# Performance work log

Hardware: AMD Instinct MI355X
Metric: run time of the kernel (lower is better)

Reference implementation:

```python
import jax, jax.numpy as jnp
import numpy as np

E, B, T, DIN, D = 8, 16, 512, 256, 256  # ensemble, batch, seq, input_dim, d_model*factor


def setup_inputs() -> dict:
    key = jax.random.key(0)
    ks = jax.random.split(key, 9)
    s_in = 1.0 / np.sqrt(DIN)
    s_d = 1.0 / np.sqrt(D)
    return {
        "x": jax.random.normal(ks[0], (E, B, T, DIN), jnp.float32),
        "hidden": jnp.zeros((1, E * B, 2 * D), jnp.float32),
        "rnn_start": (jax.random.uniform(ks[1], (B, T, 1)) < 0.02).astype(jnp.float32),
        "W_in": jax.random.normal(ks[2], (2, E, DIN, D), jnp.float32) * s_in,
        "b_in": jax.random.normal(ks[3], (2, E, D), jnp.float32) * 0.01,
        "W_mid": jax.random.normal(ks[4], (4, E, D, D), jnp.float32) * s_d,
        "b_mid": jax.random.normal(ks[5], (4, E, D), jnp.float32) * 0.01,
        "W_out": jax.random.normal(ks[6], (E, D, D), jnp.float32) * s_d,
        "b_out": jax.random.normal(ks[7], (E, D), jnp.float32) * 0.01,
    }


def _scan_tie_input_gate(v, f, h0):
    # h_t = f_t * h_{t-1} + (1 - f_t) * v_t  (tied input gate), via associative scan.
    # v, f: [N, T, D]; h0: [N, 1, D]
    b = (1.0 - f) * v

    def combine(x, y):
        a1, b1 = x
        a2, b2 = y
        return a1 * a2, a2 * b1 + b2

    A, Bc = jax.lax.associative_scan(combine, (f, b), axis=1)
    out = A * h0 + Bc  # [N, T, D]
    return out, out[:, -1:, :]


def reference(x, hidden, rnn_start, W_in, b_in, W_mid, b_mid, W_out, b_out):
    # --- first GILR stage ---
    u = jnp.einsum('ebti,meio->mebto', x, W_in) + b_in[:, :, None, None, :]
    v = jnp.tanh(u[0])
    f = jax.nn.sigmoid(u[1])
    f = f * (1.0 - rnn_start)[None]  # rnn_start [B,T,1] broadcasts over E, D

    vr = v.reshape(E * B, T, D)
    fr = f.reshape(E * B, T, D)

    h_pre, h_mid = jnp.split(hidden, 2, axis=-1)          # each [1, E*B, D]
    h_pre = jnp.transpose(h_pre, (1, 0, 2))               # [E*B, 1, D]
    h_mid = jnp.transpose(h_mid, (1, 0, 2))

    vr, h_pre_last = _scan_tie_input_gate(vr, fr, h_pre)
    v4 = vr.reshape(E, B, T, D)

    # --- LSTM-like middle stage ---
    u = jnp.einsum('ebti,meio->mebto', v4, W_mid) + b_mid[:, :, None, None, :]
    f = jax.nn.sigmoid(u[0])
    i = jax.nn.sigmoid(u[1])
    o = jax.nn.sigmoid(u[2])
    z = jnp.tanh(u[3])
    f = f * (1.0 - rnn_start)[None]

    fr = f.reshape(E * B, T, D)
    izr = (i * z).reshape(E * B, T, D)
    orr = o.reshape(E * B, T, D)

    out, h_mid_last = _scan_tie_input_gate(izr, fr, h_mid)
    out = out * orr
    out4 = out.reshape(E, B, T, D)

    # --- output projection ---
    out4 = jnp.einsum('ebti,eio->ebto', out4, W_out) + b_out[:, None, None, :]

    hidden_out = jnp.transpose(jnp.concatenate([h_pre_last, h_mid_last], axis=-1), (1, 0, 2))
    return out4, hidden_out
```

## Files before the change

### kernel.cpp

```cpp
#include <hip/hip_runtime.h>
#include <hip/hip_bf16.h>
#include <stdint.h>
#include <stddef.h>


typedef __bf16 bf16x8 __attribute__((ext_vector_type(8)));
typedef __bf16 bf16x4 __attribute__((ext_vector_type(4)));
typedef __bf16 bf16x2 __attribute__((ext_vector_type(2)));
typedef float  f32x4  __attribute__((ext_vector_type(4)));
typedef float  f32x2  __attribute__((ext_vector_type(2)));
typedef unsigned int u32x2 __attribute__((ext_vector_type(2)));

#define E_ 8
#define M_ 8192
#define K_ 256

__device__ __forceinline__ float sigm_f(float x) {
    return __builtin_amdgcn_rcpf(1.0f + __expf(-x));
}
__device__ __forceinline__ float tanh_f(float x) {
    return 1.0f - 2.0f * __builtin_amdgcn_rcpf(1.0f + __expf(2.0f * x));
}

__device__ __forceinline__ void g2lds16(const void* g, void* l) {
    __builtin_amdgcn_global_load_lds((const __attribute__((address_space(1))) void*)g,
                                     (__attribute__((address_space(3))) void*)l, 16, 0, 0);
}

template <int D>
__device__ __forceinline__ float dppshr(float x) {
    return __builtin_bit_cast(float,
        __builtin_amdgcn_update_dpp(0, __builtin_bit_cast(int, x),
                                    0x110 | D, 0xF, 0xF, true));
}

__device__ __forceinline__ void lane_scan(float& A, float& B, float& EA, float& EB, int ln15) {
    float As, Bs;
    Bs = dppshr<1>(B); As = dppshr<1>(A); B = __builtin_fmaf(A, Bs, B); A = (ln15 >= 1) ? A * As : A;
    Bs = dppshr<2>(B); As = dppshr<2>(A); B = __builtin_fmaf(A, Bs, B); A = (ln15 >= 2) ? A * As : A;
    Bs = dppshr<4>(B); As = dppshr<4>(A); B = __builtin_fmaf(A, Bs, B); A = (ln15 >= 4) ? A * As : A;
    Bs = dppshr<8>(B); As = dppshr<8>(A); B = __builtin_fmaf(A, Bs, B); A = (ln15 >= 8) ? A * As : A;
    EA = dppshr<1>(A); EA = (ln15 >= 1) ? EA : 1.0f;
    EB = dppshr<1>(B);
}

__global__ __launch_bounds__(256) void convx_k(const float* __restrict__ x, __bf16* __restrict__ xb) {
    int i = blockIdx.x * 256 + threadIdx.x;
    float4 v = ((const float4*)x)[i];
    bf16x4 o;
    o[0] = (__bf16)v.x; o[1] = (__bf16)v.y; o[2] = (__bf16)v.z; o[3] = (__bf16)v.w;
    ((bf16x4*)xb)[i] = o;
}

__global__ __launch_bounds__(256) void transw_k(const float* __restrict__ src, __bf16* __restrict__ dst,
                                                int NG, int ilv) {
    int ge = blockIdx.z;
    int g = ge >> 3, e = ge & 7;
    int k0 = blockIdx.x * 64, d0 = blockIdx.y * 64;
    __shared__ float tile[64][65];
    int t = threadIdx.x;
#pragma unroll
    for (int j = 0; j < 16; ++j) {
        int lin = j * 256 + t;
        int r = lin >> 6, c = lin & 63;
        tile[r][c] = src[((size_t)(ge * 256 + k0 + r)) * 256 + d0 + c];
    }
    __syncthreads();
#pragma unroll
    for (int j = 0; j < 16; ++j) {
        int lin = j * 256 + t;
        int r = lin >> 6, c = lin & 63;
        int d = d0 + r;
        int row = ilv ? (d * NG + g) : (g * 256 + d);
        dst[((size_t)(e * NG * 256 + row)) * K_ + k0 + c] = (__bf16)tile[c][r];
    }
}

template <int MODE, int NG>
__global__ __launch_bounds__(512, 1) void gemm_k(const __bf16* __restrict__ A,
                                                 const __bf16* __restrict__ Wt,
                                                 const float* __restrict__ bias,
                                                 const float* __restrict__ rs,
                                                 __bf16* __restrict__ gout,
                                                 float* __restrict__ fout,
                                                 const float* __restrict__ hidden,
                                                 float* __restrict__ hidout) {
    constexpr int NT  = NG * 2;
    constexpr int NMT = 2 * NT;
    const int tid = threadIdx.x;
    const int bid = blockIdx.x;
    const int e  = bid & 7;
    const int rr = bid >> 3;
    const int nt = rr & (NT - 1);
    const int ms = rr / NT;
    const int mt0 = ms * NMT;
    const int lane = tid & 63, wid = tid >> 6;
    const int wr = wid >> 2, wc = wid & 3;
    const int ln15 = lane & 15, ln16 = lane >> 4;

    __shared__ __align__(16) __bf16 As[2][32768];
    __shared__ float cAl[64], cBl[64];
    __shared__ float chL[2][64];

    bf16x8 Breg[2][8];
    {
        const __bf16* bp = Wt + ((size_t)e * (NG * 256) + nt * 128 + wc * 32 + ln15) * K_ + ln16 * 8;
#pragma unroll
        for (int j = 0; j < 2; ++j)
#pragma unroll
            for (int s = 0; s < 8; ++s)
                Breg[j][s] = *(const bf16x8*)(bp + (size_t)j * 16 * K_ + s * 32);
    }
    f32x4 bias_v[2];
#pragma unroll
    for (int j = 0; j < 2; ++j) {
        int n0 = nt * 128 + wc * 32 + j * 16 + (ln16 << 2);
        if constexpr (MODE == 0) {
#pragma unroll
            for (int q = 0; q < 4; ++q) {
                int n = n0 + q;
                bias_v[j][q] = bias[((n & 1) * E_ + e) * 256 + (n >> 1)];
            }
        } else if constexpr (MODE == 1) {
#pragma unroll
            for (int q = 0; q < 4; ++q) {
                int n = n0 + q;
                bias_v[j][q] = bias[((n & 3) * E_ + e) * 256 + (n >> 2)];
            }
        } else {
            bias_v[j] = *(const f32x4*)&bias[e * 256 + n0];
        }
    }

    const size_t Ae = ((size_t)e * M_ + (size_t)mt0 * 128) * K_;
    const int sr = tid >> 5, sr2 = sr >> 2;
    const int gg0 = (tid & 31) ^ sr2;
    const __bf16* sE = A + Ae + (size_t)sr * K_ + gg0 * 8;
    const __bf16* sO = A + Ae + (size_t)sr * K_ + (gg0 ^ 4) * 8;
    __bf16* const dbase0 = &As[0][tid * 8];
    __bf16* const dbase1 = &As[1][tid * 8];

    auto stage = [&](int tt, int buf) {
        __bf16* d = buf ? dbase1 : dbase0;
        const size_t toff = (size_t)tt * (128 * K_);
#pragma unroll
        for (int q = 0; q < 8; ++q)
            g2lds16(((q & 1) ? sO : sE) + toff + q * (16 * K_), d + q * 4096);
    };

    const int rowb = (wr * 64 + ln15 * 4) * K_;
    const int gb = ln16 ^ (lane & 7);
    const int pe_off = rowb + gb * 8;
    const int po_off = rowb + (gb ^ 4) * 8;

    f32x4 acc[4][2] = {};

    auto compute = [&](int buf) {
        const __bf16* pe = &As[0][0] + buf * 32768 + pe_off;
        const __bf16* po = &As[0][0] + buf * 32768 + po_off;
#pragma unroll
        for (int s = 0; s < 8; ++s) {
            const __bf16* p = (s & 1) ? po : pe;
            bf16x8 af[4];
#pragma unroll
            for (int i = 0; i < 4; ++i)
                af[i] = *(const bf16x8*)(p + i * K_ + (s >> 1) * 64);
#pragma unroll
            for (int i = 0; i < 4; ++i)
#pragma unroll
                for (int j = 0; j < 2; ++j)
                    acc[i][j] = __builtin_amdgcn_mfma_f32_16x16x32_bf16(Breg[j][s], af[i], acc[i][j], 0, 0, 0);
        }
    };

    stage(0, 0);
    asm volatile("s_waitcnt vmcnt(0)" ::: "memory");
    __builtin_amdgcn_s_barrier();
    __builtin_amdgcn_sched_barrier(0);

    int buf = 0;
    for (int t = 0; t < NMT; ++t) {
        const bool cs = ((t & 3) == 0);
        const int c = t >> 2;
        f32x4 rs4 = {};
        float hidv[4] = {0.f, 0.f, 0.f, 0.f};
        if constexpr (MODE != 2) {
            const int mbh = (mt0 + t) * 128 + wr * 64 + ln15 * 4;
            rs4 = *(const f32x4*)&rs[mbh];
            if constexpr (MODE == 1) {
                const int nrow = e * 16 + ms * 4 + c;
                hidv[0] = hidden[nrow * 512 + 256 + (nt * 32 + wc * 8 + 0 + ln16)];
                hidv[1] = hidden[nrow * 512 + 256 + (nt * 32 + wc * 8 + 4 + ln16)];
            } else {
                const int nrow = e * 16 + ms * 2 + c;
                f32x2 ha = *(const f32x2*)&hidden[nrow * 512 + (nt * 64 + wc * 16 + 0 + ln16 * 2)];
                f32x2 hb = *(const f32x2*)&hidden[nrow * 512 + (nt * 64 + wc * 16 + 8 + ln16 * 2)];
                hidv[0] = ha[0]; hidv[1] = ha[1]; hidv[2] = hb[0]; hidv[3] = hb[1];
            }
            __builtin_amdgcn_sched_barrier(0);
        }

        if (t + 1 < NMT) stage(t + 1, buf ^ 1);
        compute(buf);

        const int mt = mt0 + t;
        const int mb = mt * 128 + wr * 64 + ln15 * 4;

        if constexpr (MODE == 2) {
#pragma unroll
            for (int j = 0; j < 2; ++j) {
                const int n0 = nt * 128 + wc * 32 + j * 16 + (ln16 << 2);
#pragma unroll
                for (int i = 0; i < 4; ++i) {
                    f32x4 o = acc[i][j] + bias_v[j];
                    *(f32x4*)&fout[((size_t)e * M_ + mb + i) * 256 + n0] = o;
                    acc[i][j] = f32x4{};
                }
            }
        } else {
            f32x4 rsv;
#pragma unroll
            for (int q = 0; q < 4; ++q) rsv[q] = 1.0f - rs4[q];

            if constexpr (MODE == 1) {
                float PA[2][4], PB[2][4], Ov[2][4], LA[2], LB[2], EA[2], EB[2];
#pragma unroll
                for (int j = 0; j < 2; ++j) {
#pragma unroll
                    for (int i = 0; i < 4; ++i) {
                        float f  = sigm_f(acc[i][j][0] + bias_v[j][0]) * rsv[i];
                        float iv = sigm_f(acc[i][j][1] + bias_v[j][1]);
                        float o  = sigm_f(acc[i][j][2] + bias_v[j][2]);
                        float z  = tanh_f(acc[i][j][3] + bias_v[j][3]);
                        float b  = (1.0f - f) * iv * z;
                        Ov[j][i] = o;
                        if (i == 0) { PA[j][0] = f; PB[j][0] = b; }
                        else { PB[j][i] = __builtin_fmaf(f, PB[j][i - 1], b); PA[j][i] = PA[j][i - 1] * f; }
                        acc[i][j] = f32x4{};
                    }
                    LA[j] = PA[j][3]; LB[j] = PB[j][3];
                    lane_scan(LA[j], LB[j], EA[j], EB[j], ln15);
                }
                if (wr == 0 && ln15 == 15) {
#pragma unroll
                    for (int j = 0; j < 2; ++j) {
                        int sl = wc * 8 + j * 4 + ln16;
                        cAl[sl] = LA[j]; cBl[sl] = LB[j];
                    }
                }
                asm volatile("s_waitcnt lgkmcnt(0)" ::: "memory");
                __builtin_amdgcn_s_barrier();
#pragma unroll
                for (int j = 0; j < 2; ++j) {
                    const int sl = wc * 8 + j * 4 + ln16;
                    const int d = nt * 32 + wc * 8 + j * 4 + ln16;
                    float hp = cs ? hidv[j] : chL[t & 1][sl];
                    float hs = wr ? __builtin_fmaf(cAl[sl], hp, cBl[sl]) : hp;
                    float h0 = __builtin_fmaf(EA[j], hs, EB[j]);
#pragma unroll
                    for (int i = 0; i < 4; ++i) {
                        float h = __builtin_fmaf(PA[j][i], h0, PB[j][i]);
                        gout[((size_t)e * M_ + mb + i) * 256 + d] = (__bf16)(h * Ov[j][i]);
                    }
                    if (wr == 1 && ln15 == 15) {
                        float he = __builtin_fmaf(LA[j], hs, LB[j]);
                        chL[(t + 1) & 1][sl] = he;
                        if ((t & 3) == 3)
                            hidout[(e * 16 + ms * 4 + c) * 512 + 256 + d] = he;
                    }
                }
            } else {
                float PA[2][2][4], PB[2][2][4], LA[2][2], LB[2][2], EA[2][2], EB[2][2];
#pragma unroll
                for (int j = 0; j < 2; ++j) {
#pragma unroll
                    for (int dq = 0; dq < 2; ++dq) {
#pragma unroll
                        for (int i = 0; i < 4; ++i) {
                            float uv = acc[i][j][dq * 2 + 0] + bias_v[j][dq * 2 + 0];
                            float uf = acc[i][j][dq * 2 + 1] + bias_v[j][dq * 2 + 1];
                            float f = sigm_f(uf) * rsv[i];
                            float b = (1.0f - f) * tanh_f(uv);
                            if (i == 0) { PA[j][dq][0] = f; PB[j][dq][0] = b; }
                            else { PB[j][dq][i] = __builtin_fmaf(f, PB[j][dq][i - 1], b);
                                   PA[j][dq][i] = PA[j][dq][i - 1] * f; }
                        }
                        LA[j][dq] = PA[j][dq][3]; LB[j][dq] = PB[j][dq][3];
                        lane_scan(LA[j][dq], LB[j][dq], EA[j][dq], EB[j][dq], ln15);
                    }
#pragma unroll
                    for (int i = 0; i < 4; ++i) acc[i][j] = f32x4{};
                }
                if (wr == 0 && ln15 == 15) {
#pragma unroll
                    for (int j = 0; j < 2; ++j)
#pragma unroll
                        for (int dq = 0; dq < 2; ++dq) {
                            int sl = wc * 16 + j * 8 + ln16 * 2 + dq;
                            cAl[sl] = LA[j][dq]; cBl[sl] = LB[j][dq];
                        }
                }
                asm volatile("s_waitcnt lgkmcnt(0)" ::: "memory");
                __builtin_amdgcn_s_barrier();
#pragma unroll
                for (int j = 0; j < 2; ++j) {
                    const int D0 = nt * 64 + wc * 16 + j * 8 + ln16 * 2;
                    float h0q[2];
#pragma unroll
                    for (int dq = 0; dq < 2; ++dq) {
                        const int sl = wc * 16 + j * 8 + ln16 * 2 + dq;
                        float hp = cs ? hidv[j * 2 + dq] : chL[t & 1][sl];
                        float hs = wr ? __builtin_fmaf(cAl[sl], hp, cBl[sl]) : hp;
                        h0q[dq] = __builtin_fmaf(EA[j][dq], hs, EB[j][dq]);
                        if (wr == 1 && ln15 == 15) {
                            float he = __builtin_fmaf(LA[j][dq], hs, LB[j][dq]);
                            chL[(t + 1) & 1][sl] = he;
                            if ((t & 3) == 3)
                                hidout[(e * 16 + ms * 2 + c) * 512 + D0 + dq] = he;
                        }
                    }
#pragma unroll
                    for (int i = 0; i < 4; ++i) {
                        float ha = __builtin_fmaf(PA[j][0][i], h0q[0], PB[j][0][i]);
                        float hb = __builtin_fmaf(PA[j][1][i], h0q[1], PB[j][1][i]);
                        bf16x2 pk; pk[0] = (__bf16)ha; pk[1] = (__bf16)hb;
                        *(unsigned int*)&gout[((size_t)e * M_ + mb + i) * 256 + D0] =
                            __builtin_bit_cast(unsigned int, pk);
                    }
                }
            }
        }
        asm volatile("s_waitcnt vmcnt(8) lgkmcnt(0)" ::: "memory");
        __builtin_amdgcn_s_barrier();
        __builtin_amdgcn_sched_barrier(0);
        buf ^= 1;
    }
}

extern "C" void kernel_launch(void* const* d_in, const int* in_sizes, int n_in,
                              void* d_out, int out_size, void* d_ws, size_t ws_size,
                              hipStream_t stream) {
    const float* x      = (const float*)d_in[0];
    const float* hidden = (const float*)d_in[1];
    const float* rs     = (const float*)d_in[2];
    const float* W_in   = (const float*)d_in[3];
    const float* b_in   = (const float*)d_in[4];
    const float* W_mid  = (const float*)d_in[5];
    const float* b_mid  = (const float*)d_in[6];
    const float* W_out  = (const float*)d_in[7];
    const float* b_out  = (const float*)d_in[8];
    float* out = (float*)d_out;

    char* ws = (char*)d_ws;
    const size_t MiB = (size_t)1 << 20;
    __bf16* Wt1 = (__bf16*)(ws + 0);
    __bf16* Wt2 = (__bf16*)(ws + 2 * MiB);
    __bf16* Wt3 = (__bf16*)(ws + 6 * MiB);
    __bf16* v4b = (__bf16*)(ws + 8 * MiB);
    __bf16* xb  = (__bf16*)(ws + 40 * MiB);
    __bf16* G   = (__bf16*)(ws + 72 * MiB);

    float* hidout = out + (size_t)E_ * M_ * 256;

    convx_k<<<16384, 256, 0, stream>>>(x, xb);
    transw_k<<<dim3(4, 4, 16), 256, 0, stream>>>(W_in, Wt1, 2, 1);
    transw_k<<<dim3(4, 4, 32), 256, 0, stream>>>(W_mid, Wt2, 4, 1);
    transw_k<<<dim3(4, 4, 8), 256, 0, stream>>>(W_out, Wt3, 1, 0);

    gemm_k<0, 2><<<256, 512, 0, stream>>>(xb, Wt1, b_in, rs, v4b, nullptr, hidden, hidout);
    gemm_k<1, 4><<<256, 512, 0, stream>>>(v4b, Wt2, b_mid, rs, G, nullptr, hidden, hidout);
    gemm_k<2, 1><<<256, 512, 0, stream>>>(G, Wt3, b_out, nullptr, nullptr, out, nullptr, nullptr);
}
```

Measured before the change: 178.9 us.

## Reshape warp tiling to 4x2 grid with 32-row, 64-col per-warp tiles

Changes the 8-warp layout from 2 row-groups by 4 column-groups to 4 row-groups by 2 column-groups. Each warp now covers 32 rows and 64 columns, holding twice as many weight registers (Breg 4x8) and loading half as many A fragments from LDS per step. The cross-warp scan carry becomes a 3-stage chain through per-row-group LDS slots instead of a single combine. The LDS swizzle is redone to match. This cuts LDS A-fragment traffic per MFMA, but raises register pressure and lengthens the sequential carry chain across warps.

```diff
diff --git a/kernel.cpp b/kernel.cpp
--- a/kernel.cpp
+++ b/kernel.cpp
@@ -9,7 +9,6 @@
 typedef __bf16 bf16x2 __attribute__((ext_vector_type(2)));
 typedef float  f32x4  __attribute__((ext_vector_type(4)));
 typedef float  f32x2  __attribute__((ext_vector_type(2)));
-typedef unsigned int u32x2 __attribute__((ext_vector_type(2)));
 
 #define E_ 8
 #define M_ 8192
@@ -95,26 +94,26 @@
     const int ms = rr / NT;
     const int mt0 = ms * NMT;
     const int lane = tid & 63, wid = tid >> 6;
-    const int wr = wid >> 2, wc = wid & 3;
+    const int wr = wid >> 1, wc = wid & 1;
     const int ln15 = lane & 15, ln16 = lane >> 4;
 
     __shared__ __align__(16) __bf16 As[2][32768];
-    __shared__ float cAl[64], cBl[64];
+    __shared__ float cAl[3][64], cBl[3][64];
     __shared__ float chL[2][64];
 
-    bf16x8 Breg[2][8];
+    bf16x8 Breg[4][8];
     {
-        const __bf16* bp = Wt + ((size_t)e * (NG * 256) + nt * 128 + wc * 32 + ln15) * K_ + ln16 * 8;
-#pragma unroll
-        for (int j = 0; j < 2; ++j)
+        const __bf16* bp = Wt + ((size_t)e * (NG * 256) + nt * 128 + wc * 64 + ln15) * K_ + ln16 * 8;
+#pragma unroll
+        for (int j = 0; j < 4; ++j)
 #pragma unroll
             for (int s = 0; s < 8; ++s)
                 Breg[j][s] = *(const bf16x8*)(bp + (size_t)j * 16 * K_ + s * 32);
     }
-    f32x4 bias_v[2];
-#pragma unroll
-    for (int j = 0; j < 2; ++j) {
-        int n0 = nt * 128 + wc * 32 + j * 16 + (ln16 << 2);
+    f32x4 bias_v[4];
+#pragma unroll
+    for (int j = 0; j < 4; ++j) {
+        int n0 = nt * 128 + wc * 64 + j * 16 + (ln16 << 2);
         if constexpr (MODE == 0) {
 #pragma unroll
             for (int q = 0; q < 4; ++q) {
@@ -148,12 +147,12 @@
             g2lds16(((q & 1) ? sO : sE) + toff + q * (16 * K_), d + q * 4096);
     };
 
-    const int rowb = (wr * 64 + ln15 * 4) * K_;
-    const int gb = ln16 ^ (lane & 7);
-    const int pe_off = rowb + gb * 8;
-    const int po_off = rowb + (gb ^ 4) * 8;
-
-    f32x4 acc[4][2] = {};
+    const int rowb = (wr * 32 + ln15 * 2) * K_;
+    const int key = ln15 >> 1;
+    const int pe_off = rowb + (ln16 ^ key) * 8;
+    const int po_off = rowb + ((4 | ln16) ^ key) * 8;
+
+    f32x4 acc[2][4] = {};
 
     auto compute = [&](int buf) {
         const __bf16* pe = &As[0][0] + buf * 32768 + pe_off;
@@ -161,14 +160,14 @@
 #pragma unroll
         for (int s = 0; s < 8; ++s) {
             const __bf16* p = (s & 1) ? po : pe;
-            bf16x8 af[4];
-#pragma unroll
-            for (int i = 0; i < 4; ++i)
+            bf16x8 af[2];
+#pragma unroll
+            for (int i = 0; i < 2; ++i)
                 af[i] = *(const bf16x8*)(p + i * K_ + (s >> 1) * 64);
 #pragma unroll
-            for (int i = 0; i < 4; ++i)
-#pragma unroll
-                for (int j = 0; j < 2; ++j)
+            for (int i = 0; i < 2; ++i)
+#pragma unroll
+                for (int j = 0; j < 4; ++j)
                     acc[i][j] = __builtin_amdgcn_mfma_f32_16x16x32_bf16(Breg[j][s], af[i], acc[i][j], 0, 0, 0);
         }
     };
@@ -182,20 +181,23 @@
     for (int t = 0; t < NMT; ++t) {
         const bool cs = ((t & 3) == 0);
         const int c = t >> 2;
-        f32x4 rs4 = {};
-        float hidv[4] = {0.f, 0.f, 0.f, 0.f};
+        f32x2 rs2 = {};
+        float hidv[8];
         if constexpr (MODE != 2) {
-            const int mbh = (mt0 + t) * 128 + wr * 64 + ln15 * 4;
-            rs4 = *(const f32x4*)&rs[mbh];
+            const int mbh = (mt0 + t) * 128 + wr * 32 + ln15 * 2;
+            rs2 = *(const f32x2*)&rs[mbh];
             if constexpr (MODE == 1) {
                 const int nrow = e * 16 + ms * 4 + c;
-                hidv[0] = hidden[nrow * 512 + 256 + (nt * 32 + wc * 8 + 0 + ln16)];
-                hidv[1] = hidden[nrow * 512 + 256 + (nt * 32 + wc * 8 + 4 + ln16)];
+#pragma unroll
+                for (int j = 0; j < 4; ++j)
+                    hidv[j] = hidden[nrow * 512 + 256 + (nt * 32 + wc * 16 + j * 4 + ln16)];
             } else {
                 const int nrow = e * 16 + ms * 2 + c;
-                f32x2 ha = *(const f32x2*)&hidden[nrow * 512 + (nt * 64 + wc * 16 + 0 + ln16 * 2)];
-                f32x2 hb = *(const f32x2*)&hidden[nrow * 512 + (nt * 64 + wc * 16 + 8 + ln16 * 2)];
-                hidv[0] = ha[0]; hidv[1] = ha[1]; hidv[2] = hb[0]; hidv[3] = hb[1];
+#pragma unroll
+                for (int j = 0; j < 4; ++j) {
+                    f32x2 hv = *(const f32x2*)&hidden[nrow * 512 + (nt * 64 + wc * 32 + j * 8 + ln16 * 2)];
+                    hidv[j * 2] = hv[0]; hidv[j * 2 + 1] = hv[1];
+                }
             }
             __builtin_amdgcn_sched_barrier(0);
         }
@@ -204,30 +206,29 @@
         compute(buf);
 
         const int mt = mt0 + t;
-        const int mb = mt * 128 + wr * 64 + ln15 * 4;
+        const int mb = mt * 128 + wr * 32 + ln15 * 2;
 
         if constexpr (MODE == 2) {
 #pragma unroll
-            for (int j = 0; j < 2; ++j) {
-                const int n0 = nt * 128 + wc * 32 + j * 16 + (ln16 << 2);
-#pragma unroll
-                for (int i = 0; i < 4; ++i) {
+            for (int j = 0; j < 4; ++j) {
+                const int n0 = nt * 128 + wc * 64 + j * 16 + (ln16 << 2);
+#pragma unroll
+                for (int i = 0; i < 2; ++i) {
                     f32x4 o = acc[i][j] + bias_v[j];
                     *(f32x4*)&fout[((size_t)e * M_ + mb + i) * 256 + n0] = o;
                     acc[i][j] = f32x4{};
                 }
             }
         } else {
-            f32x4 rsv;
-#pragma unroll
-            for (int q = 0; q < 4; ++q) rsv[q] = 1.0f - rs4[q];
+            float rsv[2];
+            rsv[0] = 1.0f - rs2[0]; rsv[1] = 1.0f - rs2[1];
 
             if constexpr (MODE == 1) {
-                float PA[2][4], PB[2][4], Ov[2][4], LA[2], LB[2], EA[2], EB[2];
-#pragma unroll
-                for (int j = 0; j < 2; ++j) {
-#pragma unroll
-                    for (int i = 0; i < 4; ++i) {
+                float PA[4][2], PB[4][2], Ov[4][2], LA[4], LB[4], EA[4], EB[4];
+#pragma unroll
+                for (int j = 0; j < 4; ++j) {
+#pragma unroll
+                    for (int i = 0; i < 2; ++i) {
                         float f  = sigm_f(acc[i][j][0] + bias_v[j][0]) * rsv[i];
                         float iv = sigm_f(acc[i][j][1] + bias_v[j][1]);
                         float o  = sigm_f(acc[i][j][2] + bias_v[j][2]);
@@ -235,92 +236,96 @@
                         float b  = (1.0f - f) * iv * z;
                         Ov[j][i] = o;
                         if (i == 0) { PA[j][0] = f; PB[j][0] = b; }
-                        else { PB[j][i] = __builtin_fmaf(f, PB[j][i - 1], b); PA[j][i] = PA[j][i - 1] * f; }
+                        else { PB[j][1] = __builtin_fmaf(f, PB[j][0], b); PA[j][1] = PA[j][0] * f; }
                         acc[i][j] = f32x4{};
                     }
-                    LA[j] = PA[j][3]; LB[j] = PB[j][3];
+                    LA[j] = PA[j][1]; LB[j] = PB[j][1];
                     lane_scan(LA[j], LB[j], EA[j], EB[j], ln15);
                 }
-                if (wr == 0 && ln15 == 15) {
-#pragma unroll
-                    for (int j = 0; j < 2; ++j) {
-                        int sl = wc * 8 + j * 4 + ln16;
-                        cAl[sl] = LA[j]; cBl[sl] = LB[j];
+                if (wr < 3 && ln15 == 15) {
+#pragma unroll
+                    for (int j = 0; j < 4; ++j) {
+                        int dl = wc * 16 + j * 4 + ln16;
+                        cAl[wr][dl] = LA[j]; cBl[wr][dl] = LB[j];
                     }
                 }
                 asm volatile("s_waitcnt lgkmcnt(0)" ::: "memory");
                 __builtin_amdgcn_s_barrier();
 #pragma unroll
-                for (int j = 0; j < 2; ++j) {
-                    const int sl = wc * 8 + j * 4 + ln16;
-                    const int d = nt * 32 + wc * 8 + j * 4 + ln16;
-                    float hp = cs ? hidv[j] : chL[t & 1][sl];
-                    float hs = wr ? __builtin_fmaf(cAl[sl], hp, cBl[sl]) : hp;
+                for (int j = 0; j < 4; ++j) {
+                    const int dl = wc * 16 + j * 4 + ln16;
+                    const int d = nt * 32 + dl;
+                    float hs = cs ? hidv[j] : chL[t & 1][dl];
+                    if (wr > 0) hs = __builtin_fmaf(cAl[0][dl], hs, cBl[0][dl]);
+                    if (wr > 1) hs = __builtin_fmaf(cAl[1][dl], hs, cBl[1][dl]);
+                    if (wr > 2) hs = __builtin_fmaf(cAl[2][dl], hs, cBl[2][dl]);
                     float h0 = __builtin_fmaf(EA[j], hs, EB[j]);
 #pragma unroll
-                    for (int i = 0; i < 4; ++i) {
+                    for (int i = 0; i < 2; ++i) {
                         float h = __builtin_fmaf(PA[j][i], h0, PB[j][i]);
                         gout[((size_t)e * M_ + mb + i) * 256 + d] = (__bf16)(h * Ov[j][i]);
                     }
-                    if (wr == 1 && ln15 == 15) {
+                    if (wr == 3 && ln15 == 15) {
                         float he = __builtin_fmaf(LA[j], hs, LB[j]);
-                        chL[(t + 1) & 1][sl] = he;
+                        chL[(t + 1) & 1][dl] = he;
                         if ((t & 3) == 3)
                             hidout[(e * 16 + ms * 4 + c) * 512 + 256 + d] = he;
                     }
                 }
             } else {
-                float PA[2][2][4], PB[2][2][4], LA[2][2], LB[2][2], EA[2][2], EB[2][2];
-#pragma unroll
-                for (int j = 0; j < 2; ++j) {
+                float PA[4][2][2], PB[4][2][2], LA[4][2], LB[4][2], EA[4][2], EB[4][2];
+#pragma unroll
+                for (int j = 0; j < 4; ++j) {
 #pragma unroll
                     for (int dq = 0; dq < 2; ++dq) {
 #pragma unroll
-                        for (int i = 0; i < 4; ++i) {
+                        for (int i = 0; i < 2; ++i) {
                             float uv = acc[i][j][dq * 2 + 0] + bias_v[j][dq * 2 + 0];
                             float uf = acc[i][j][dq * 2 + 1] + bias_v[j][dq * 2 + 1];
                             float f = sigm_f(uf) * rsv[i];
                             float b = (1.0f - f) * tanh_f(uv);
                             if (i == 0) { PA[j][dq][0] = f; PB[j][dq][0] = b; }
-                            else { PB[j][dq][i] = __builtin_fmaf(f, PB[j][dq][i - 1], b);
-                                   PA[j][dq][i] = PA[j][dq][i - 1] * f; }
+                            else { PB[j][dq][1] = __builtin_fmaf(f, PB[j][dq][0], b);
+                                   PA[j][dq][1] = PA[j][dq][0] * f; }
                         }
-                        LA[j][dq] = PA[j][dq][3]; LB[j][dq] = PB[j][dq][3];
+                        LA[j][dq] = PA[j][dq][1]; LB[j][dq] = PB[j][dq][1];
                         lane_scan(LA[j][dq], LB[j][dq], EA[j][dq], EB[j][dq], ln15);
                     }
 #pragma unroll
-                    for (int i = 0; i < 4; ++i) acc[i][j] = f32x4{};
-                }
-                if (wr == 0 && ln15 == 15) {
-#pragma unroll
-                    for (int j = 0; j < 2; ++j)
+                    for (int i = 0; i < 2; ++i) acc[i][j] = f32x4{};
+                }
+                if (wr < 3 && ln15 == 15) {
+#pragma unroll
+                    for (int j = 0; j < 4; ++j)
 #pragma unroll
                         for (int dq = 0; dq < 2; ++dq) {
-                            int sl = wc * 16 + j * 8 + ln16 * 2 + dq;
-                            cAl[sl] = LA[j][dq]; cBl[sl] = LB[j][dq];
+                            int dl = wc * 32 + j * 8 + ln16 * 2 + dq;
+                            cAl[wr][dl] = LA[j][dq]; cBl[wr][dl] = LB[j][dq];
                         }
                 }
                 asm volatile("s_waitcnt lgkmcnt(0)" ::: "memory");
                 __builtin_amdgcn_s_barrier();
 #pragma unroll
-                for (int j = 0; j < 2; ++j) {
-                    const int D0 = nt * 64 + wc * 16 + j * 8 + ln16 * 2;
+                for (int j = 0; j < 4; ++j) {
+                    const int D0 = nt * 64 + wc * 32 + j * 8 + ln16 * 2;
                     float h0q[2];
 #pragma unroll
                     for (int dq = 0; dq < 2; ++dq) {
-                        const int sl = wc * 16 + j * 8 + ln16 * 2 + dq;
-                        float hp = cs ? hidv[j * 2 + dq] : chL[t & 1][sl];
-                        float hs = wr ? __builtin_fmaf(cAl[sl], hp, cBl[sl]) : hp;
+                        const int dl = wc * 32 + j * 8 + ln16 * 2 + dq;
+                        float hs = cs ? hidv[j * 2 + dq] : chL[t & 1][dl];
+                        if (wr > 0) hs = __builtin_fmaf(cAl[0][dl], hs, cBl[0][dl]);
+                        if (wr > 1) hs = __builtin_fmaf(cAl[1][dl], hs, cBl[1][dl]);
+                        if (wr > 2) hs = __builtin_fmaf(cAl[2][dl], hs, cBl[2][dl]);
                         h0q[dq] = __builtin_fmaf(EA[j][dq], hs, EB[j][dq]);
-                        if (wr == 1 && ln15 == 15) {
+                        if (wr == 3 && ln15 == 15) {
                             float he = __builtin_fmaf(LA[j][dq], hs, LB[j][dq]);
-                            chL[(t + 1) & 1][sl] = he;
+                            chL[(t + 1) & 1][dl] = he;
                             if ((t & 3) == 3)
                                 hidout[(e * 16 + ms * 2 + c) * 512 + D0 + dq] = he;
                         }
                     }
 #pragma unroll
-                    for (int i = 0; i < 4; ++i) {
+                    for (int i = 0; i < 2; ++i) {
                         float ha = __builtin_fmaf(PA[j][0][i], h0q[0], PB[j][0][i]);
                         float hb = __builtin_fmaf(PA[j][1][i], h0q[1], PB[j][1][i]);
                         bf16x2 pk; pk[0] = (__bf16)ha; pk[1] = (__bf16)hb;
```

Result: slower. 186.8 us (+4.4%).

## Software-pipeline scan epilogue behind next tile's MFMA using double accumulators

Applied to the files above, without the earlier changes.

For the two scan modes, the loop now keeps two accumulator sets and runs the gate/scan epilogue of tile t-1 after issuing the MFMA compute for tile t. The goal is to let the transcendental and scan arithmetic overlap with matrix-core work instead of running serially after each tile. A final epilogue handles the last tile. This doubles the accumulator register footprint, which may raise register pressure and lower occupancy, and it assumes NMT is even.

```diff
diff --git a/kernel.cpp b/kernel.cpp
--- a/kernel.cpp
+++ b/kernel.cpp
@@ -9,7 +9,6 @@
 typedef __bf16 bf16x2 __attribute__((ext_vector_type(2)));
 typedef float  f32x4  __attribute__((ext_vector_type(4)));
 typedef float  f32x2  __attribute__((ext_vector_type(2)));
-typedef unsigned int u32x2 __attribute__((ext_vector_type(2)));
 
 #define E_ 8
 #define M_ 8192
@@ -153,9 +152,7 @@
     const int pe_off = rowb + gb * 8;
     const int po_off = rowb + (gb ^ 4) * 8;
 
-    f32x4 acc[4][2] = {};
-
-    auto compute = [&](int buf) {
+    auto compute = [&](f32x4 (&acc)[4][2], int buf) {
         const __bf16* pe = &As[0][0] + buf * 32768 + pe_off;
         const __bf16* po = &As[0][0] + buf * 32768 + po_off;
 #pragma unroll
@@ -178,35 +175,13 @@
     __builtin_amdgcn_s_barrier();
     __builtin_amdgcn_sched_barrier(0);
 
-    int buf = 0;
-    for (int t = 0; t < NMT; ++t) {
-        const bool cs = ((t & 3) == 0);
-        const int c = t >> 2;
-        f32x4 rs4 = {};
-        float hidv[4] = {0.f, 0.f, 0.f, 0.f};
-        if constexpr (MODE != 2) {
-            const int mbh = (mt0 + t) * 128 + wr * 64 + ln15 * 4;
-            rs4 = *(const f32x4*)&rs[mbh];
-            if constexpr (MODE == 1) {
-                const int nrow = e * 16 + ms * 4 + c;
-                hidv[0] = hidden[nrow * 512 + 256 + (nt * 32 + wc * 8 + 0 + ln16)];
-                hidv[1] = hidden[nrow * 512 + 256 + (nt * 32 + wc * 8 + 4 + ln16)];
-            } else {
-                const int nrow = e * 16 + ms * 2 + c;
-                f32x2 ha = *(const f32x2*)&hidden[nrow * 512 + (nt * 64 + wc * 16 + 0 + ln16 * 2)];
-                f32x2 hb = *(const f32x2*)&hidden[nrow * 512 + (nt * 64 + wc * 16 + 8 + ln16 * 2)];
-                hidv[0] = ha[0]; hidv[1] = ha[1]; hidv[2] = hb[0]; hidv[3] = hb[1];
-            }
-            __builtin_amdgcn_sched_barrier(0);
-        }
-
-        if (t + 1 < NMT) stage(t + 1, buf ^ 1);
-        compute(buf);
-
-        const int mt = mt0 + t;
-        const int mb = mt * 128 + wr * 64 + ln15 * 4;
-
-        if constexpr (MODE == 2) {
+    if constexpr (MODE == 2) {
+        f32x4 acc[4][2] = {};
+        int buf = 0;
+        for (int t = 0; t < NMT; ++t) {
+            if (t + 1 < NMT) stage(t + 1, buf ^ 1);
+            compute(acc, buf);
+            const int mb = (mt0 + t) * 128 + wr * 64 + ln15 * 4;
 #pragma unroll
             for (int j = 0; j < 2; ++j) {
                 const int n0 = nt * 128 + wc * 32 + j * 16 + (ln16 << 2);
@@ -217,10 +192,20 @@
                     acc[i][j] = f32x4{};
                 }
             }
-        } else {
+            asm volatile("s_waitcnt vmcnt(8) lgkmcnt(0)" ::: "memory");
+            __builtin_amdgcn_s_barrier();
+            __builtin_amdgcn_sched_barrier(0);
+            buf ^= 1;
+        }
+        return;
+    } else {
+        auto do_epi = [&](f32x4 (&acc)[4][2], int tp, const f32x4& rs4p, const float* hidvp) {
+            const bool cs = ((tp & 3) == 0);
+            const int c = tp >> 2;
+            const int mb = (mt0 + tp) * 128 + wr * 64 + ln15 * 4;
             f32x4 rsv;
 #pragma unroll
-            for (int q = 0; q < 4; ++q) rsv[q] = 1.0f - rs4[q];
+            for (int q = 0; q < 4; ++q) rsv[q] = 1.0f - rs4p[q];
 
             if constexpr (MODE == 1) {
                 float PA[2][4], PB[2][4], Ov[2][4], LA[2], LB[2], EA[2], EB[2];
@@ -254,7 +239,7 @@
                 for (int j = 0; j < 2; ++j) {
                     const int sl = wc * 8 + j * 4 + ln16;
                     const int d = nt * 32 + wc * 8 + j * 4 + ln16;
-                    float hp = cs ? hidv[j] : chL[t & 1][sl];
+                    float hp = cs ? hidvp[j] : chL[tp & 1][sl];
                     float hs = wr ? __builtin_fmaf(cAl[sl], hp, cBl[sl]) : hp;
                     float h0 = __builtin_fmaf(EA[j], hs, EB[j]);
 #pragma unroll
@@ -264,8 +249,8 @@
                     }
                     if (wr == 1 && ln15 == 15) {
                         float he = __builtin_fmaf(LA[j], hs, LB[j]);
-                        chL[(t + 1) & 1][sl] = he;
-                        if ((t & 3) == 3)
+                        chL[(tp + 1) & 1][sl] = he;
+                        if ((tp & 3) == 3)
                             hidout[(e * 16 + ms * 4 + c) * 512 + 256 + d] = he;
                     }
                 }
@@ -309,13 +294,13 @@
 #pragma unroll
                     for (int dq = 0; dq < 2; ++dq) {
                         const int sl = wc * 16 + j * 8 + ln16 * 2 + dq;
-                        float hp = cs ? hidv[j * 2 + dq] : chL[t & 1][sl];
+                        float hp = cs ? hidvp[j * 2 + dq] : chL[tp & 1][sl];
                         float hs = wr ? __builtin_fmaf(cAl[sl], hp, cBl[sl]) : hp;
                         h0q[dq] = __builtin_fmaf(EA[j][dq], hs, EB[j][dq]);
                         if (wr == 1 && ln15 == 15) {
                             float he = __builtin_fmaf(LA[j][dq], hs, LB[j][dq]);
-                            chL[(t + 1) & 1][sl] = he;
-                            if ((t & 3) == 3)
+                            chL[(tp + 1) & 1][sl] = he;
+                            if ((tp & 3) == 3)
                                 hidout[(e * 16 + ms * 2 + c) * 512 + D0 + dq] = he;
                         }
                     }
@@ -329,11 +314,54 @@
                     }
                 }
             }
+        };
+
+        f32x4 accA[4][2] = {}, accB[4][2] = {};
+        f32x4 rs4_p = {};
+        float hidv_p[4] = {0.f, 0.f, 0.f, 0.f};
+        int buf = 0;
+
+        auto iter = [&](int t, f32x4 (&accC)[4][2], f32x4 (&accP)[4][2]) {
+            const int c = t >> 2;
+            f32x4 rs4_n;
+            float hidv_n[4] = {0.f, 0.f, 0.f, 0.f};
+            {
+                const int mbh = (mt0 + t) * 128 + wr * 64 + ln15 * 4;
+                rs4_n = *(const f32x4*)&rs[mbh];
+                if constexpr (MODE == 1) {
+                    const int nrow = e * 16 + ms * 4 + c;
+                    hidv_n[0] = hidden[nrow * 512 + 256 + (nt * 32 + wc * 8 + 0 + ln16)];
+                    hidv_n[1] = hidden[nrow * 512 + 256 + (nt * 32 + wc * 8 + 4 + ln16)];
+                } else {
+                    const int nrow = e * 16 + ms * 2 + c;
+                    f32x2 ha = *(const f32x2*)&hidden[nrow * 512 + (nt * 64 + wc * 16 + 0 + ln16 * 2)];
+                    f32x2 hb = *(const f32x2*)&hidden[nrow * 512 + (nt * 64 + wc * 16 + 8 + ln16 * 2)];
+                    hidv_n[0] = ha[0]; hidv_n[1] = ha[1]; hidv_n[2] = hb[0]; hidv_n[3] = hb[1];
+                }
+                __builtin_amdgcn_sched_barrier(0);
+            }
+            if (t + 1 < NMT) stage(t + 1, buf ^ 1);
+            compute(accC, buf);
+            if (t > 0) do_epi(accP, t - 1, rs4_p, hidv_p);
+            if (t == 0) {
+                asm volatile("s_waitcnt vmcnt(0) lgkmcnt(0)" ::: "memory");
+            } else {
+                asm volatile("s_waitcnt vmcnt(8) lgkmcnt(0)" ::: "memory");
+            }
+            __builtin_amdgcn_s_barrier();
+            __builtin_amdgcn_sched_barrier(0);
+            buf ^= 1;
+            rs4_p = rs4_n;
+#pragma unroll
+            for (int q = 0; q < 4; ++q) hidv_p[q] = hidv_n[q];
+        };
+
+#pragma unroll 1
+        for (int t2 = 0; t2 < NMT; t2 += 2) {
+            iter(t2, accA, accB);
+            iter(t2 + 1, accB, accA);
         }
-        asm volatile("s_waitcnt vmcnt(8) lgkmcnt(0)" ::: "memory");
-        __builtin_amdgcn_s_barrier();
-        __builtin_amdgcn_sched_barrier(0);
-        buf ^= 1;
+        do_epi(accB, NMT - 1, rs4_p, hidv_p);
     }
 }
 
```

After: 170.9 us. -4.5%, faster.

## Double per-block N tile to 256 columns, halving A-tile restaging

Applied to the files above, without the earlier changes.

Each block now covers 256 output columns (four 16-wide MFMA column groups per wave) instead of 128, so the number of N tiles per expert halves. Each row block of A is staged into LDS half as many times and reused across twice as many MFMAs. The M-tiles per block change with it, and the scan bookkeeping, hidden-state indexing and carry arrays are widened to match. In exchange, register pressure roughly doubles (B fragments, accumulators, scan temporaries) and there are fewer blocks to fill the CUs.

```diff
diff --git a/kernel.cpp b/kernel.cpp
--- a/kernel.cpp
+++ b/kernel.cpp
@@ -9,7 +9,6 @@
 typedef __bf16 bf16x2 __attribute__((ext_vector_type(2)));
 typedef float  f32x4  __attribute__((ext_vector_type(4)));
 typedef float  f32x2  __attribute__((ext_vector_type(2)));
-typedef unsigned int u32x2 __attribute__((ext_vector_type(2)));
 
 #define E_ 8
 #define M_ 8192
@@ -85,13 +84,13 @@
                                                  float* __restrict__ fout,
                                                  const float* __restrict__ hidden,
                                                  float* __restrict__ hidout) {
-    constexpr int NT  = NG * 2;
-    constexpr int NMT = 2 * NT;
+    constexpr int NT  = NG;
+    constexpr int NMT = 2 * NG;
     const int tid = threadIdx.x;
     const int bid = blockIdx.x;
     const int e  = bid & 7;
     const int rr = bid >> 3;
-    const int nt = rr & (NT - 1);
+    const int nt = rr % NT;
     const int ms = rr / NT;
     const int mt0 = ms * NMT;
     const int lane = tid & 63, wid = tid >> 6;
@@ -99,22 +98,22 @@
     const int ln15 = lane & 15, ln16 = lane >> 4;
 
     __shared__ __align__(16) __bf16 As[2][32768];
-    __shared__ float cAl[64], cBl[64];
-    __shared__ float chL[2][64];
-
-    bf16x8 Breg[2][8];
+    __shared__ float cAl[128], cBl[128];
+    __shared__ float chL[2][128];
+
+    bf16x8 Breg[4][8];
     {
-        const __bf16* bp = Wt + ((size_t)e * (NG * 256) + nt * 128 + wc * 32 + ln15) * K_ + ln16 * 8;
-#pragma unroll
-        for (int j = 0; j < 2; ++j)
+        const __bf16* bp = Wt + ((size_t)e * (NG * 256) + nt * 256 + wc * 64 + ln15) * K_ + ln16 * 8;
+#pragma unroll
+        for (int j = 0; j < 4; ++j)
 #pragma unroll
             for (int s = 0; s < 8; ++s)
                 Breg[j][s] = *(const bf16x8*)(bp + (size_t)j * 16 * K_ + s * 32);
     }
-    f32x4 bias_v[2];
-#pragma unroll
-    for (int j = 0; j < 2; ++j) {
-        int n0 = nt * 128 + wc * 32 + j * 16 + (ln16 << 2);
+    f32x4 bias_v[4];
+#pragma unroll
+    for (int j = 0; j < 4; ++j) {
+        int n0 = nt * 256 + wc * 64 + j * 16 + (ln16 << 2);
         if constexpr (MODE == 0) {
 #pragma unroll
             for (int q = 0; q < 4; ++q) {
@@ -153,7 +152,7 @@
     const int pe_off = rowb + gb * 8;
     const int po_off = rowb + (gb ^ 4) * 8;
 
-    f32x4 acc[4][2] = {};
+    f32x4 acc[4][4] = {};
 
     auto compute = [&](int buf) {
         const __bf16* pe = &As[0][0] + buf * 32768 + pe_off;
@@ -168,7 +167,7 @@
 #pragma unroll
             for (int i = 0; i < 4; ++i)
 #pragma unroll
-                for (int j = 0; j < 2; ++j)
+                for (int j = 0; j < 4; ++j)
                     acc[i][j] = __builtin_amdgcn_mfma_f32_16x16x32_bf16(Breg[j][s], af[i], acc[i][j], 0, 0, 0);
         }
     };
@@ -181,21 +180,22 @@
     int buf = 0;
     for (int t = 0; t < NMT; ++t) {
         const bool cs = ((t & 3) == 0);
-        const int c = t >> 2;
+        const int nrow = e * 16 + ((mt0 + t) >> 2);
         f32x4 rs4 = {};
-        float hidv[4] = {0.f, 0.f, 0.f, 0.f};
+        float hidv[8];
         if constexpr (MODE != 2) {
             const int mbh = (mt0 + t) * 128 + wr * 64 + ln15 * 4;
             rs4 = *(const f32x4*)&rs[mbh];
             if constexpr (MODE == 1) {
-                const int nrow = e * 16 + ms * 4 + c;
-                hidv[0] = hidden[nrow * 512 + 256 + (nt * 32 + wc * 8 + 0 + ln16)];
-                hidv[1] = hidden[nrow * 512 + 256 + (nt * 32 + wc * 8 + 4 + ln16)];
+#pragma unroll
+                for (int j = 0; j < 4; ++j)
+                    hidv[j] = hidden[nrow * 512 + 256 + (nt * 64 + wc * 16 + j * 4 + ln16)];
             } else {
-                const int nrow = e * 16 + ms * 2 + c;
-                f32x2 ha = *(const f32x2*)&hidden[nrow * 512 + (nt * 64 + wc * 16 + 0 + ln16 * 2)];
-                f32x2 hb = *(const f32x2*)&hidden[nrow * 512 + (nt * 64 + wc * 16 + 8 + ln16 * 2)];
-                hidv[0] = ha[0]; hidv[1] = ha[1]; hidv[2] = hb[0]; hidv[3] = hb[1];
+#pragma unroll
+                for (int j = 0; j < 4; ++j) {
+                    f32x2 hv = *(const f32x2*)&hidden[nrow * 512 + (nt * 128 + wc * 32 + j * 8 + ln16 * 2)];
+                    hidv[j * 2] = hv[0]; hidv[j * 2 + 1] = hv[1];
+                }
             }
             __builtin_amdgcn_sched_barrier(0);
         }
@@ -208,8 +208,8 @@
 
         if constexpr (MODE == 2) {
 #pragma unroll
-            for (int j = 0; j < 2; ++j) {
-                const int n0 = nt * 128 + wc * 32 + j * 16 + (ln16 << 2);
+            for (int j = 0; j < 4; ++j) {
+                const int n0 = nt * 256 + wc * 64 + j * 16 + (ln16 << 2);
 #pragma unroll
                 for (int i = 0; i < 4; ++i) {
                     f32x4 o = acc[i][j] + bias_v[j];
@@ -223,9 +223,9 @@
             for (int q = 0; q < 4; ++q) rsv[q] = 1.0f - rs4[q];
 
             if constexpr (MODE == 1) {
-                float PA[2][4], PB[2][4], Ov[2][4], LA[2], LB[2], EA[2], EB[2];
-#pragma unroll
-                for (int j = 0; j < 2; ++j) {
+                float PA[4][4], PB[4][4], Ov[4][4], LA[4], LB[4], EA[4], EB[4];
+#pragma unroll
+                for (int j = 0; j < 4; ++j) {
 #pragma unroll
                     for (int i = 0; i < 4; ++i) {
                         float f  = sigm_f(acc[i][j][0] + bias_v[j][0]) * rsv[i];
@@ -243,17 +243,17 @@
                 }
                 if (wr == 0 && ln15 == 15) {
 #pragma unroll
-                    for (int j = 0; j < 2; ++j) {
-                        int sl = wc * 8 + j * 4 + ln16;
+                    for (int j = 0; j < 4; ++j) {
+                        int sl = wc * 16 + j * 4 + ln16;
                         cAl[sl] = LA[j]; cBl[sl] = LB[j];
                     }
                 }
                 asm volatile("s_waitcnt lgkmcnt(0)" ::: "memory");
                 __builtin_amdgcn_s_barrier();
 #pragma unroll
-                for (int j = 0; j < 2; ++j) {
-                    const int sl = wc * 8 + j * 4 + ln16;
-                    const int d = nt * 32 + wc * 8 + j * 4 + ln16;
+                for (int j = 0; j < 4; ++j) {
+                    const int sl = wc * 16 + j * 4 + ln16;
+                    const int d = nt * 64 + sl;
                     float hp = cs ? hidv[j] : chL[t & 1][sl];
                     float hs = wr ? __builtin_fmaf(cAl[sl], hp, cBl[sl]) : hp;
                     float h0 = __builtin_fmaf(EA[j], hs, EB[j]);
@@ -266,13 +266,13 @@
                         float he = __builtin_fmaf(LA[j], hs, LB[j]);
                         chL[(t + 1) & 1][sl] = he;
                         if ((t & 3) == 3)
-                            hidout[(e * 16 + ms * 4 + c) * 512 + 256 + d] = he;
+                            hidout[nrow * 512 + 256 + d] = he;
                     }
                 }
             } else {
-                float PA[2][2][4], PB[2][2][4], LA[2][2], LB[2][2], EA[2][2], EB[2][2];
-#pragma unroll
-                for (int j = 0; j < 2; ++j) {
+                float PA[4][2][4], PB[4][2][4], LA[4][2], LB[4][2], EA[4][2], EB[4][2];
+#pragma unroll
+                for (int j = 0; j < 4; ++j) {
 #pragma unroll
                     for (int dq = 0; dq < 2; ++dq) {
 #pragma unroll
@@ -293,22 +293,22 @@
                 }
                 if (wr == 0 && ln15 == 15) {
 #pragma unroll
-                    for (int j = 0; j < 2; ++j)
+                    for (int j = 0; j < 4; ++j)
 #pragma unroll
                         for (int dq = 0; dq < 2; ++dq) {
-                            int sl = wc * 16 + j * 8 + ln16 * 2 + dq;
+                            int sl = wc * 32 + j * 8 + ln16 * 2 + dq;
                             cAl[sl] = LA[j][dq]; cBl[sl] = LB[j][dq];
                         }
                 }
                 asm volatile("s_waitcnt lgkmcnt(0)" ::: "memory");
                 __builtin_amdgcn_s_barrier();
 #pragma unroll
-                for (int j = 0; j < 2; ++j) {
-                    const int D0 = nt * 64 + wc * 16 + j * 8 + ln16 * 2;
+                for (int j = 0; j < 4; ++j) {
+                    const int D0 = nt * 128 + wc * 32 + j * 8 + ln16 * 2;
                     float h0q[2];
 #pragma unroll
                     for (int dq = 0; dq < 2; ++dq) {
-                        const int sl = wc * 16 + j * 8 + ln16 * 2 + dq;
+                        const int sl = wc * 32 + j * 8 + ln16 * 2 + dq;
                         float hp = cs ? hidv[j * 2 + dq] : chL[t & 1][sl];
                         float hs = wr ? __builtin_fmaf(cAl[sl], hp, cBl[sl]) : hp;
                         h0q[dq] = __builtin_fmaf(EA[j][dq], hs, EB[j][dq]);
@@ -316,7 +316,7 @@
                             float he = __builtin_fmaf(LA[j][dq], hs, LB[j][dq]);
                             chL[(t + 1) & 1][sl] = he;
                             if ((t & 3) == 3)
-                                hidout[(e * 16 + ms * 2 + c) * 512 + D0 + dq] = he;
+                                hidout[nrow * 512 + D0 + dq] = he;
                         }
                     }
 #pragma unroll
@@ -330,7 +330,7 @@
                 }
             }
         }
-        asm volatile("s_waitcnt vmcnt(8) lgkmcnt(0)" ::: "memory");
+        asm volatile("s_waitcnt vmcnt(16) lgkmcnt(0)" ::: "memory");
         __builtin_amdgcn_s_barrier();
         __builtin_amdgcn_sched_barrier(0);
         buf ^= 1;
```

Result: slower. 205.6 us (+15.0%).
